# Performance work log

Measured on AMD Instinct MI355X. Metric: run time of the kernel, lower is better.

The kernel has to match this reference:

```python
import jax, jax.numpy as jnp
import numpy as np

N_Q = 16384; N_S = 16384; NN = 32; F_IN = 128; F_OUT = 256
K = 15; DIM = 3
RADIUS = 10.0
KP_EXTENT_CFG = 1.0      # config.NETWORK.KP_EXTENT (also scales learned offsets)
DENSITY = 5.0            # config.NETWORK.DENSITY_PARAMETER
EXTENT = KP_EXTENT_CFG * RADIUS / DENSITY   # 2.0
K_RADIUS = 1.5 * EXTENT
OFFSET_DIM = DIM * (K - 1)  # modulated=False, version=0 -> 42


def setup_inputs() -> dict:
    key = jax.random.key(0)
    ks = jax.random.split(key, 8)
    query_points = jax.random.uniform(ks[0], (N_Q, DIM), dtype=jnp.float32)
    support_points = jax.random.uniform(ks[1], (N_S, DIM), dtype=jnp.float32)
    neighbors = jax.random.randint(ks[2], (N_Q, NN), 0, N_S)
    features = jax.random.normal(ks[3], (N_S, F_IN), dtype=jnp.float32)
    # kernel points: fixed disposition inside ball of radius 1.5*extent, first point at center
    kp = jax.random.normal(ks[4], (K, DIM), dtype=jnp.float32)
    kp = kp / jnp.linalg.norm(kp, axis=1, keepdims=True) * (0.7 * K_RADIUS)
    K_points = kp.at[0].set(0.0)
    weight = jax.random.normal(ks[5], (K, F_IN, F_OUT), dtype=jnp.float32) / np.sqrt(F_IN)
    deformable_weight = jax.random.normal(ks[6], (K, F_IN, OFFSET_DIM), dtype=jnp.float32) / np.sqrt(F_IN)
    bias = jnp.zeros((OFFSET_DIM,), dtype=jnp.float32)
    return {"query_points": query_points, "support_points": support_points,
            "neighbors": neighbors, "features": features, "K_points": K_points,
            "weight": weight, "deformable_weight": deformable_weight, "bias": bias}


def _gather_neighb(query_points, support_points, neighbors, features):
    # pad with shadow point (far away) and zero feature row, as in KPConv_ops
    sp = jnp.concatenate([support_points, jnp.full((1, DIM), 1e6, support_points.dtype)], 0)
    ft = jnp.concatenate([features, jnp.zeros((1, features.shape[1]), features.dtype)], 0)
    rel = sp[neighbors] - query_points[:, None, :]   # [n, nn, 3]
    nfeat = ft[neighbors]                            # [n, nn, f]
    return rel, nfeat


def _linear_influence(sq_dist):
    # KP_INFLUENCE='linear': relu(1 - d/extent); CONVOLUTION_MODE='sum'
    return jnp.maximum(1.0 - jnp.sqrt(sq_dist) / EXTENT, 0.0)


def reference(query_points, support_points, neighbors, features, K_points,
              weight, deformable_weight, bias):
    rel, nfeat = _gather_neighb(query_points, support_points, neighbors, features)

    # --- rigid KPConv producing offsets (version=0) ---
    d0 = rel[:, :, None, :] - K_points[None, None, :, :]   # [n, nn, K, 3]
    sq0 = jnp.sum(d0 * d0, axis=-1)                        # [n, nn, K]
    w0 = _linear_influence(sq0)
    wf0 = jnp.einsum('enk,enf->ekf', w0, nfeat)            # [n, K, f]
    feat0 = jnp.einsum('ekf,kfo->eo', wf0, deformable_weight) + bias  # [n, 42]

    # not modulated: reshape to offsets, prepend zero offset for center kernel point
    offsets = feat0.reshape(-1, K - 1, DIM)
    offsets = jnp.concatenate([jnp.zeros_like(offsets[:, :1, :]), offsets], axis=1)
    offsets = offsets * KP_EXTENT_CFG                      # [n, K, 3]

    # --- deformable KPConv ---
    def_kp = K_points[None, :, :] + offsets                # [n, K, 3]
    d1 = rel[:, :, None, :] - def_kp[:, None, :, :]        # [n, nn, K, 3]
    sq1 = jnp.sum(d1 * d1, axis=-1)                        # [n, nn, K]
    w1 = _linear_influence(sq1)                            # out-of-range neighbors get 0 weight
    wf1 = jnp.einsum('enk,enf->ekf', w1, nfeat)            # [n, K, f]
    out = jnp.einsum('ekf,kfo->eo', wf1, weight)           # [n, f_out]
    return out
```

## Files before the change

kernel.cpp:

```cpp
#include <hip/hip_runtime.h>
#include <hip/hip_bf16.h>
#include <math.h>

typedef __attribute__((ext_vector_type(8))) short bf16x8;
typedef __attribute__((ext_vector_type(4))) float f32x4;

#define NQ 16384
#define NN 32
#define FI 128
#define FO 256
#define KPN 15
#define OD 42
#define INV_EXT 0.5f

#define KT2 64
#define WST 2048

#define SWZ(row, blk) (((blk) ^ ((row) & 7)) << 5)

#define WS_FP1    0u
#define WS_FP2    (8u * 1024u * 1024u)
#define WS_BSW    (12u * 1024u * 1024u)
#define WS_DWBH   (13u * 1024u * 1024u)
#define WS_DWBL   (WS_DWBH + 196608u)
#define WS_DEFKP  (14u * 1024u * 1024u)

static __device__ __forceinline__ unsigned short f2bf(float x) {
    union { __hip_bfloat16 h; unsigned short u; } cv;
    cv.h = __float2bfloat16(x);
    return cv.u;
}
static __device__ __forceinline__ float bf2f(unsigned short h) {
    union { unsigned int u; float f; } cv;
    cv.u = ((unsigned int)h) << 16;
    return cv.f;
}

__global__ void pre_all(const float* __restrict__ feat,
                        unsigned int* __restrict__ fp1, unsigned int* __restrict__ fp2,
                        const float* __restrict__ w, unsigned short* __restrict__ Bsw,
                        const float* __restrict__ dw,
                        unsigned short* __restrict__ dhi, unsigned short* __restrict__ dlo)
{
    const int b = blockIdx.x, t = threadIdx.x;
    if (b < 4096) {
        const int tid = b * 256 + t;
        const int s = tid >> 6, r = tid & 63;
        const int fp = r >> 4, low = r & 15;
        const float a = feat[s * FI + fp * 32 + low];
        const float c = feat[s * FI + fp * 32 + 16 + low];
        const unsigned short ha = f2bf(a), hc = f2bf(c);
        const unsigned int w0 = (unsigned int)ha | ((unsigned int)hc << 16);
        const unsigned int w1 = (unsigned int)f2bf(a - bf2f(ha)) |
                                ((unsigned int)f2bf(c - bf2f(hc)) << 16);
        uint2 pr; pr.x = w0; pr.y = w1;
        *(uint2*)&fp1[s * 128 + fp * 32 + low * 2] = pr;
        fp2[s * 64 + fp * 16 + low] = w0;
    } else if (b < 4096 + 256) {
        const int tid = (b - 4096) * 256 + t;
        const int lane = tid & 63;
        const int kt   = (tid >> 6) & 63;
        const int nt   = tid >> 12;
        const int n    = nt * 16 + (lane & 15);
        const int kbase = kt * 32 + (lane >> 4) * 8;
        unsigned int p[4];
        #pragma unroll
        for (int jj = 0; jj < 4; jj++) {
            unsigned int lo, hi;
            {
                const int kk = kbase + 2 * jj;
                const int f = kk >> 4, k = kk & 15;
                lo = (k < KPN) ? f2bf(w[(k * FI + f) * FO + n]) : 0u;
            }
            {
                const int kk = kbase + 2 * jj + 1;
                const int f = kk >> 4, k = kk & 15;
                hi = (k < KPN) ? f2bf(w[(k * FI + f) * FO + n]) : 0u;
            }
            p[jj] = lo | (hi << 16);
        }
        unsigned int* op = (unsigned int*)&Bsw[tid * 8];
        op[0] = p[0]; op[1] = p[1]; op[2] = p[2]; op[3] = p[3];
    } else {
        const int tid = (b - 4352) * 256 + t;
        const int lane = tid & 63;
        const int kt   = (tid >> 6) & 63;
        const int nt   = tid >> 12;
        const int o    = nt * 16 + (lane & 15);
        const int kbase = kt * 32 + (lane >> 4) * 8;
        #pragma unroll
        for (int j = 0; j < 8; j++) {
            const int kf = kbase + j;
            const int f = kf >> 4, k = kf & 15;
            float v = (k < KPN && o < OD) ? dw[(k * FI + f) * OD + o] : 0.f;
            unsigned short h = f2bf(v);
            dhi[tid * 8 + j] = h;
            dlo[tid * 8 + j] = f2bf(v - bf2f(h));
        }
    }
}

__global__ __launch_bounds__(512, 4)
void k1_offsets(const float* __restrict__ query, const float* __restrict__ support,
                const int* __restrict__ neighbors, const unsigned int* __restrict__ fp1,
                const float* __restrict__ kpoints,
                const unsigned short* __restrict__ dwB_hi,
                const unsigned short* __restrict__ dwB_lo,
                const float* __restrict__ bias, float* __restrict__ defkp)
{
    __shared__ unsigned short wfA_hi[8 * WST];
    __shared__ unsigned short wfA_lo[8 * WST];
    __shared__ float relx[256], rely[256], relz[256];
    __shared__ int   nbr_s[256];
    __shared__ float kp_s[48];
    __shared__ f32x4 cred[3 * 64];

    const int t = threadIdx.x;
    const int qbase = blockIdx.x * 8;
    if (t < 45) kp_s[t] = kpoints[t];
    if (t >= 45 && t < 48) kp_s[t] = 0.f;

    if (t < 256) {
        const int e = t >> 5, n = t & 31;
        const int q = qbase + e;
        const int idx = neighbors[q * NN + n];
        nbr_s[t] = idx;
        relx[t] = support[idx * 3 + 0] - query[q * 3 + 0];
        rely[t] = support[idx * 3 + 1] - query[q * 3 + 1];
        relz[t] = support[idx * 3 + 2] - query[q * 3 + 2];
    }
    __syncthreads();

    const int wave = t >> 6, lane = t & 63;
    const int quad = lane >> 4, low = lane & 15;

    {
        const int ee = wave;
        const int kb = (low < KPN) ? low * 3 : 0;
        const float kx = kp_s[kb + 0], ky = kp_s[kb + 1], kz = kp_s[kb + 2];
        union { unsigned short u[8]; bf16x8 v; } ah, al;
        int rows[8];
        #pragma unroll
        for (int j = 0; j < 8; j++) {
            const int ni = ee * 32 + quad * 8 + j;
            rows[j] = nbr_s[ni];
            const float dx = relx[ni] - kx;
            const float dy = rely[ni] - ky;
            const float dz = relz[ni] - kz;
            const float d = sqrtf(dx * dx + dy * dy + dz * dz);
            float w = 1.0f - d * INV_EXT;
            w = (low < KPN && w > 0.f) ? w : 0.f;
            const unsigned short h = f2bf(w);
            ah.u[j] = h;
            al.u[j] = f2bf(w - bf2f(h));
        }
        #pragma unroll
        for (int fp = 0; fp < 4; fp++) {
            union { unsigned int u[4]; bf16x8 v; } bhA, blA, bhB, blB;
            #pragma unroll
            for (int jj = 0; jj < 4; jj++) {
                const uint2 d0 = *(const uint2*)&fp1[rows[2 * jj] * 128 + fp * 32 + low * 2];
                const uint2 d1 = *(const uint2*)&fp1[rows[2 * jj + 1] * 128 + fp * 32 + low * 2];
                bhA.u[jj] = __builtin_amdgcn_perm(d1.x, d0.x, 0x05040100u);
                bhB.u[jj] = __builtin_amdgcn_perm(d1.x, d0.x, 0x07060302u);
                blA.u[jj] = __builtin_amdgcn_perm(d1.y, d0.y, 0x05040100u);
                blB.u[jj] = __builtin_amdgcn_perm(d1.y, d0.y, 0x07060302u);
            }
            #pragma unroll
            for (int hh2 = 0; hh2 < 2; hh2++) {
                const bf16x8 bh = hh2 ? bhB.v : bhA.v;
                const bf16x8 bl = hh2 ? blB.v : blA.v;
                const int ft = fp * 2 + hh2;
                f32x4 acc = {0.f, 0.f, 0.f, 0.f};
                acc = __builtin_amdgcn_mfma_f32_16x16x32_bf16(al.v, bh, acc, 0, 0, 0);
                acc = __builtin_amdgcn_mfma_f32_16x16x32_bf16(ah.v, bl, acc, 0, 0, 0);
                acc = __builtin_amdgcn_mfma_f32_16x16x32_bf16(ah.v, bh, acc, 0, 0, 0);
                const int col  = ft * 16 + low;
                const int base = ee * WST + SWZ(ee, col >> 1) + ((col & 1) << 4) + quad * 4;
                const unsigned short h0 = f2bf(acc[0]), h1 = f2bf(acc[1]);
                const unsigned short h2 = f2bf(acc[2]), h3 = f2bf(acc[3]);
                unsigned int* ph = (unsigned int*)&wfA_hi[base];
                ph[0] = (unsigned int)h0 | ((unsigned int)h1 << 16);
                ph[1] = (unsigned int)h2 | ((unsigned int)h3 << 16);
                unsigned int* pl = (unsigned int*)&wfA_lo[base];
                pl[0] = (unsigned int)f2bf(acc[0] - bf2f(h0)) |
                        ((unsigned int)f2bf(acc[1] - bf2f(h1)) << 16);
                pl[1] = (unsigned int)f2bf(acc[2] - bf2f(h2)) |
                        ((unsigned int)f2bf(acc[3] - bf2f(h3)) << 16);
            }
        }
    }
    __syncthreads();

    f32x4 acc = {0.f, 0.f, 0.f, 0.f};
    const int nt = wave >> 1, half = wave & 1;
    if (wave < 6) {
        const bf16x8* Bh = (const bf16x8*)dwB_hi;
        const bf16x8* Bl = (const bf16x8*)dwB_lo;
        const int rl = low & 7;
        const int arow = rl * WST;
        const int kt0 = half * 32;
        #pragma unroll 2
        for (int kt = kt0; kt < kt0 + 32; kt++) {
            const int ao = arow + SWZ(rl, kt) + quad * 8;
            bf16x8 a_h = *(const bf16x8*)&wfA_hi[ao];
            bf16x8 a_l = *(const bf16x8*)&wfA_lo[ao];
            bf16x8 b_h = Bh[(nt * KT2 + kt) * 64 + lane];
            bf16x8 b_l = Bl[(nt * KT2 + kt) * 64 + lane];
            acc = __builtin_amdgcn_mfma_f32_16x16x32_bf16(a_l, b_h, acc, 0, 0, 0);
            acc = __builtin_amdgcn_mfma_f32_16x16x32_bf16(a_h, b_l, acc, 0, 0, 0);
            acc = __builtin_amdgcn_mfma_f32_16x16x32_bf16(a_h, b_h, acc, 0, 0, 0);
        }
        if (half == 1) cred[nt * 64 + lane] = acc;
    } else if (wave == 6 && lane < 24) {
        defkp[(qbase + lane / 3) * 45 + (lane % 3)] = kp_s[lane % 3];
    }
    __syncthreads();

    if (wave < 6 && half == 0) {
        f32x4 o2 = cred[nt * 64 + lane];
        acc[0] += o2[0]; acc[1] += o2[1]; acc[2] += o2[2]; acc[3] += o2[3];
        const int o = nt * 16 + low;
        if (quad < 2 && o < OD) {
            const float bo = bias[o] + kp_s[3 + o];
            #pragma unroll
            for (int r = 0; r < 4; r++) {
                const int ee = quad * 4 + r;
                defkp[(qbase + ee) * 45 + 3 + o] = bo + acc[r];
            }
        }
    }
}

__global__ __launch_bounds__(512, 4)
void k2_deform(const float* __restrict__ query, const float* __restrict__ support,
               const int* __restrict__ neighbors, const unsigned int* __restrict__ fp2,
               const unsigned short* __restrict__ Bsw, const float* __restrict__ defkp,
               float* __restrict__ out)
{
    __shared__ unsigned short wfA[16 * WST];
    __shared__ float relx[512], rely[512], relz[512];
    __shared__ float dk_s[16 * 45];
    __shared__ int   nbr_s[512];

    const int t = threadIdx.x;
    const int qbase = blockIdx.x * 16;

    for (int i = t; i < 16 * 45; i += 512) dk_s[i] = defkp[qbase * 45 + i];

    const int e = t >> 5, n = t & 31;
    const int q = qbase + e;
    const int idx = neighbors[q * NN + n];
    nbr_s[t] = idx;
    relx[t] = support[idx * 3 + 0] - query[q * 3 + 0];
    rely[t] = support[idx * 3 + 1] - query[q * 3 + 1];
    relz[t] = support[idx * 3 + 2] - query[q * 3 + 2];
    __syncthreads();

    const int wave = t >> 6, lane = t & 63;
    const int quad = lane >> 4, low = lane & 15;

    {
        const int kb = (low < KPN) ? low * 3 : 0;
        for (int ei = 0; ei < 2; ei++) {
            const int ee = wave * 2 + ei;
            const float kx = dk_s[ee * 45 + kb + 0];
            const float ky = dk_s[ee * 45 + kb + 1];
            const float kz = dk_s[ee * 45 + kb + 2];
            union { unsigned short u[8]; bf16x8 v; } a;
            int rows[8];
            #pragma unroll
            for (int j = 0; j < 8; j++) {
                const int ni = ee * 32 + quad * 8 + j;
                rows[j] = nbr_s[ni];
                const float dx = relx[ni] - kx;
                const float dy = rely[ni] - ky;
                const float dz = relz[ni] - kz;
                const float d = sqrtf(dx * dx + dy * dy + dz * dz);
                float w = 1.0f - d * INV_EXT;
                w = (low < KPN && w > 0.f) ? w : 0.f;
                a.u[j] = f2bf(w);
            }
            #pragma unroll
            for (int fp = 0; fp < 4; fp++) {
                union { unsigned int u[4]; bf16x8 v; } bA, bB;
                #pragma unroll
                for (int jj = 0; jj < 4; jj++) {
                    const unsigned int d0 = fp2[rows[2 * jj] * 64 + fp * 16 + low];
                    const unsigned int d1 = fp2[rows[2 * jj + 1] * 64 + fp * 16 + low];
                    bA.u[jj] = __builtin_amdgcn_perm(d1, d0, 0x05040100u);
                    bB.u[jj] = __builtin_amdgcn_perm(d1, d0, 0x07060302u);
                }
                #pragma unroll
                for (int hh2 = 0; hh2 < 2; hh2++) {
                    const bf16x8 b = hh2 ? bB.v : bA.v;
                    const int ft = fp * 2 + hh2;
                    f32x4 acc = {0.f, 0.f, 0.f, 0.f};
                    acc = __builtin_amdgcn_mfma_f32_16x16x32_bf16(a.v, b, acc, 0, 0, 0);
                    const int col  = ft * 16 + low;
                    const int base = ee * WST + SWZ(ee, col >> 1) + ((col & 1) << 4) + quad * 4;
                    unsigned int* wp = (unsigned int*)&wfA[base];
                    wp[0] = (unsigned int)f2bf(acc[0]) | ((unsigned int)f2bf(acc[1]) << 16);
                    wp[1] = (unsigned int)f2bf(acc[2]) | ((unsigned int)f2bf(acc[3]) << 16);
                }
            }
        }
    }
    __syncthreads();

    {
        const int nt0 = wave * 2, nt1 = nt0 + 1;
        f32x4 acc0 = {0.f, 0.f, 0.f, 0.f}, acc1 = {0.f, 0.f, 0.f, 0.f};
        const bf16x8* Bp = (const bf16x8*)Bsw;
        const int arow = low * WST;
        #pragma unroll 4
        for (int kt = 0; kt < KT2; kt++) {
            bf16x8 a  = *(const bf16x8*)&wfA[arow + SWZ(low, kt) + quad * 8];
            bf16x8 b0 = Bp[(nt0 * KT2 + kt) * 64 + lane];
            bf16x8 b1 = Bp[(nt1 * KT2 + kt) * 64 + lane];
            acc0 = __builtin_amdgcn_mfma_f32_16x16x32_bf16(a, b0, acc0, 0, 0, 0);
            acc1 = __builtin_amdgcn_mfma_f32_16x16x32_bf16(a, b1, acc1, 0, 0, 0);
        }
        #pragma unroll
        for (int r = 0; r < 4; r++) {
            const int ee = quad * 4 + r;
            out[(qbase + ee) * FO + nt0 * 16 + low] = acc0[r];
            out[(qbase + ee) * FO + nt1 * 16 + low] = acc1[r];
        }
    }
}

extern "C" void kernel_launch(void* const* d_in, const int* in_sizes, int n_in,
                              void* d_out, int out_size, void* d_ws, size_t ws_size,
                              hipStream_t stream) {
    const float* query     = (const float*)d_in[0];
    const float* support   = (const float*)d_in[1];
    const int*   neighbors = (const int*)  d_in[2];
    const float* features  = (const float*)d_in[3];
    const float* kpoints   = (const float*)d_in[4];
    const float* weight    = (const float*)d_in[5];
    const float* dweight   = (const float*)d_in[6];
    const float* bias      = (const float*)d_in[7];
    float*       out       = (float*)d_out;

    char* ws = (char*)d_ws;
    unsigned int*   fp1  = (unsigned int*)(ws + WS_FP1);
    unsigned int*   fp2  = (unsigned int*)(ws + WS_FP2);
    unsigned short* Bsw  = (unsigned short*)(ws + WS_BSW);
    unsigned short* dwBh = (unsigned short*)(ws + WS_DWBH);
    unsigned short* dwBl = (unsigned short*)(ws + WS_DWBL);
    float*          defkp = (float*)(ws + WS_DEFKP);

    pre_all<<<4400, 256, 0, stream>>>(features, fp1, fp2, weight, Bsw,
                                      dweight, dwBh, dwBl);
    k1_offsets<<<NQ / 8, 512, 0, stream>>>(query, support, neighbors, fp1,
                                           kpoints, dwBh, dwBl, bias, defkp);
    k2_deform<<<NQ / 16, 512, 0, stream>>>(query, support, neighbors, fp2,
                                           Bsw, defkp, out);
}
```

Measured before the change: 190.8 us.

## Double queries per block and chunk the K-dimension through shared memory

Both the offset and deformable kernels now handle twice as many query points per block (16 and 32). The weighted-feature A tile is produced and consumed in four K-chunks with a new transposed, XOR-swizzled LDS layout, so the LDS footprint stays bounded while each weight B-fragment loaded from global memory is reused across more query rows. In the deform kernel every wave now uses the full 16-row MFMA M dimension twice instead of padding, and neighbor indices are stored as 16-bit values. The cost is extra barriers per chunk, more registers for the additional accumulators, and fewer blocks in flight.

```diff
diff --git a/kernel.cpp b/kernel.cpp
--- a/kernel.cpp
+++ b/kernel.cpp
@@ -13,11 +13,6 @@
 #define OD 42
 #define INV_EXT 0.5f
 
-#define KT2 64
-#define WST 2048
-
-#define SWZ(row, blk) (((blk) ^ ((row) & 7)) << 5)
-
 #define WS_FP1    0u
 #define WS_FP2    (8u * 1024u * 1024u)
 #define WS_BSW    (12u * 1024u * 1024u)
@@ -35,6 +30,8 @@
     cv.u = ((unsigned int)h) << 16;
     return cv.f;
 }
+
+union U8 { unsigned short u[8]; bf16x8 v; };
 
 __global__ void pre_all(const float* __restrict__ feat,
                         unsigned int* __restrict__ fp1, unsigned int* __restrict__ fp2,
@@ -108,19 +105,19 @@
                 const unsigned short* __restrict__ dwB_lo,
                 const float* __restrict__ bias, float* __restrict__ defkp)
 {
-    __shared__ unsigned short wfA_hi[8 * WST];
-    __shared__ unsigned short wfA_lo[8 * WST];
-    __shared__ float relx[256], rely[256], relz[256];
-    __shared__ int   nbr_s[256];
+    __shared__ unsigned short wfA_hi[8192];
+    __shared__ unsigned short wfA_lo[8192];
+    __shared__ float relx[512], rely[512], relz[512];
+    __shared__ int   nbr_s[512];
     __shared__ float kp_s[48];
     __shared__ f32x4 cred[3 * 64];
 
     const int t = threadIdx.x;
-    const int qbase = blockIdx.x * 8;
+    const int qbase = blockIdx.x * 16;
     if (t < 45) kp_s[t] = kpoints[t];
     if (t >= 45 && t < 48) kp_s[t] = 0.f;
 
-    if (t < 256) {
+    {
         const int e = t >> 5, n = t & 31;
         const int q = qbase + e;
         const int idx = neighbors[q * NN + n];
@@ -133,17 +130,16 @@
 
     const int wave = t >> 6, lane = t & 63;
     const int quad = lane >> 4, low = lane & 15;
-
-    {
-        const int ee = wave;
-        const int kb = (low < KPN) ? low * 3 : 0;
-        const float kx = kp_s[kb + 0], ky = kp_s[kb + 1], kz = kp_s[kb + 2];
-        union { unsigned short u[8]; bf16x8 v; } ah, al;
-        int rows[8];
+    const int ee0 = wave * 2;
+
+    const int kb = (low < KPN) ? low * 3 : 0;
+    const float kx = kp_s[kb + 0], ky = kp_s[kb + 1], kz = kp_s[kb + 2];
+    U8 ah[2], al[2];
+    #pragma unroll
+    for (int ei = 0; ei < 2; ei++) {
         #pragma unroll
         for (int j = 0; j < 8; j++) {
-            const int ni = ee * 32 + quad * 8 + j;
-            rows[j] = nbr_s[ni];
+            const int ni = (ee0 + ei) * 32 + quad * 8 + j;
             const float dx = relx[ni] - kx;
             const float dy = rely[ni] - ky;
             const float dz = relz[ni] - kz;
@@ -151,16 +147,25 @@
             float w = 1.0f - d * INV_EXT;
             w = (low < KPN && w > 0.f) ? w : 0.f;
             const unsigned short h = f2bf(w);
-            ah.u[j] = h;
-            al.u[j] = f2bf(w - bf2f(h));
-        }
-        #pragma unroll
-        for (int fp = 0; fp < 4; fp++) {
+            ah[ei].u[j] = h;
+            al[ei].u[j] = f2bf(w - bf2f(h));
+        }
+    }
+
+    f32x4 acc = {0.f, 0.f, 0.f, 0.f};
+    const int nt = wave >> 1, half = wave & 1;
+
+    for (int c = 0; c < 4; c++) {
+        #pragma unroll
+        for (int ei = 0; ei < 2; ei++) {
+            const int ee = ee0 + ei;
             union { unsigned int u[4]; bf16x8 v; } bhA, blA, bhB, blB;
             #pragma unroll
             for (int jj = 0; jj < 4; jj++) {
-                const uint2 d0 = *(const uint2*)&fp1[rows[2 * jj] * 128 + fp * 32 + low * 2];
-                const uint2 d1 = *(const uint2*)&fp1[rows[2 * jj + 1] * 128 + fp * 32 + low * 2];
+                const int r0 = nbr_s[ee * 32 + quad * 8 + 2 * jj];
+                const int r1 = nbr_s[ee * 32 + quad * 8 + 2 * jj + 1];
+                const uint2 d0 = *(const uint2*)&fp1[r0 * 128 + c * 32 + low * 2];
+                const uint2 d1 = *(const uint2*)&fp1[r1 * 128 + c * 32 + low * 2];
                 bhA.u[jj] = __builtin_amdgcn_perm(d1.x, d0.x, 0x05040100u);
                 bhB.u[jj] = __builtin_amdgcn_perm(d1.x, d0.x, 0x07060302u);
                 blA.u[jj] = __builtin_amdgcn_perm(d1.y, d0.y, 0x05040100u);
@@ -170,58 +175,56 @@
             for (int hh2 = 0; hh2 < 2; hh2++) {
                 const bf16x8 bh = hh2 ? bhB.v : bhA.v;
                 const bf16x8 bl = hh2 ? blB.v : blA.v;
-                const int ft = fp * 2 + hh2;
-                f32x4 acc = {0.f, 0.f, 0.f, 0.f};
-                acc = __builtin_amdgcn_mfma_f32_16x16x32_bf16(al.v, bh, acc, 0, 0, 0);
-                acc = __builtin_amdgcn_mfma_f32_16x16x32_bf16(ah.v, bl, acc, 0, 0, 0);
-                acc = __builtin_amdgcn_mfma_f32_16x16x32_bf16(ah.v, bh, acc, 0, 0, 0);
-                const int col  = ft * 16 + low;
-                const int base = ee * WST + SWZ(ee, col >> 1) + ((col & 1) << 4) + quad * 4;
-                const unsigned short h0 = f2bf(acc[0]), h1 = f2bf(acc[1]);
-                const unsigned short h2 = f2bf(acc[2]), h3 = f2bf(acc[3]);
-                unsigned int* ph = (unsigned int*)&wfA_hi[base];
-                ph[0] = (unsigned int)h0 | ((unsigned int)h1 << 16);
-                ph[1] = (unsigned int)h2 | ((unsigned int)h3 << 16);
-                unsigned int* pl = (unsigned int*)&wfA_lo[base];
-                pl[0] = (unsigned int)f2bf(acc[0] - bf2f(h0)) |
-                        ((unsigned int)f2bf(acc[1] - bf2f(h1)) << 16);
-                pl[1] = (unsigned int)f2bf(acc[2] - bf2f(h2)) |
-                        ((unsigned int)f2bf(acc[3] - bf2f(h3)) << 16);
-            }
-        }
-    }
+                f32x4 o = {0.f, 0.f, 0.f, 0.f};
+                o = __builtin_amdgcn_mfma_f32_16x16x32_bf16(al[ei].v, bh, o, 0, 0, 0);
+                o = __builtin_amdgcn_mfma_f32_16x16x32_bf16(ah[ei].v, bl, o, 0, 0, 0);
+                o = __builtin_amdgcn_mfma_f32_16x16x32_bf16(ah[ei].v, bh, o, 0, 0, 0);
+                const int cblk = (hh2 * 16 + low) * 2 + (quad >> 1);
+                const int hw = cblk * 128 + ((ee ^ (cblk & 15)) * 8) + (quad & 1) * 4;
+                const unsigned short h0 = f2bf(o[0]), h1 = f2bf(o[1]);
+                const unsigned short h2 = f2bf(o[2]), h3 = f2bf(o[3]);
+                uint2 ph;
+                ph.x = (unsigned int)h0 | ((unsigned int)h1 << 16);
+                ph.y = (unsigned int)h2 | ((unsigned int)h3 << 16);
+                *(uint2*)&wfA_hi[hw] = ph;
+                uint2 pl;
+                pl.x = (unsigned int)f2bf(o[0] - bf2f(h0)) |
+                       ((unsigned int)f2bf(o[1] - bf2f(h1)) << 16);
+                pl.y = (unsigned int)f2bf(o[2] - bf2f(h2)) |
+                       ((unsigned int)f2bf(o[3] - bf2f(h3)) << 16);
+                *(uint2*)&wfA_lo[hw] = pl;
+            }
+        }
+        __syncthreads();
+        if (wave < 6) {
+            const bf16x8* Bh = (const bf16x8*)dwB_hi;
+            const bf16x8* Bl = (const bf16x8*)dwB_lo;
+            #pragma unroll 4
+            for (int ktl = half * 8; ktl < half * 8 + 8; ktl++) {
+                const int cblk = ktl * 4 + quad;
+                const int hw = cblk * 128 + ((low ^ (cblk & 15)) * 8);
+                bf16x8 a_h = *(const bf16x8*)&wfA_hi[hw];
+                bf16x8 a_l = *(const bf16x8*)&wfA_lo[hw];
+                const int ktg = c * 16 + ktl;
+                bf16x8 b_h = Bh[(nt * 64 + ktg) * 64 + lane];
+                bf16x8 b_l = Bl[(nt * 64 + ktg) * 64 + lane];
+                acc = __builtin_amdgcn_mfma_f32_16x16x32_bf16(a_l, b_h, acc, 0, 0, 0);
+                acc = __builtin_amdgcn_mfma_f32_16x16x32_bf16(a_h, b_l, acc, 0, 0, 0);
+                acc = __builtin_amdgcn_mfma_f32_16x16x32_bf16(a_h, b_h, acc, 0, 0, 0);
+            }
+        } else if (c == 0 && wave == 6 && lane < 48) {
+            defkp[(qbase + lane / 3) * 45 + (lane % 3)] = kp_s[lane % 3];
+        }
+        __syncthreads();
+    }
+
+    if (wave < 6 && half == 1) cred[nt * 64 + lane] = acc;
     __syncthreads();
-
-    f32x4 acc = {0.f, 0.f, 0.f, 0.f};
-    const int nt = wave >> 1, half = wave & 1;
-    if (wave < 6) {
-        const bf16x8* Bh = (const bf16x8*)dwB_hi;
-        const bf16x8* Bl = (const bf16x8*)dwB_lo;
-        const int rl = low & 7;
-        const int arow = rl * WST;
-        const int kt0 = half * 32;
-        #pragma unroll 2
-        for (int kt = kt0; kt < kt0 + 32; kt++) {
-            const int ao = arow + SWZ(rl, kt) + quad * 8;
-            bf16x8 a_h = *(const bf16x8*)&wfA_hi[ao];
-            bf16x8 a_l = *(const bf16x8*)&wfA_lo[ao];
-            bf16x8 b_h = Bh[(nt * KT2 + kt) * 64 + lane];
-            bf16x8 b_l = Bl[(nt * KT2 + kt) * 64 + lane];
-            acc = __builtin_amdgcn_mfma_f32_16x16x32_bf16(a_l, b_h, acc, 0, 0, 0);
-            acc = __builtin_amdgcn_mfma_f32_16x16x32_bf16(a_h, b_l, acc, 0, 0, 0);
-            acc = __builtin_amdgcn_mfma_f32_16x16x32_bf16(a_h, b_h, acc, 0, 0, 0);
-        }
-        if (half == 1) cred[nt * 64 + lane] = acc;
-    } else if (wave == 6 && lane < 24) {
-        defkp[(qbase + lane / 3) * 45 + (lane % 3)] = kp_s[lane % 3];
-    }
-    __syncthreads();
-
     if (wave < 6 && half == 0) {
         f32x4 o2 = cred[nt * 64 + lane];
         acc[0] += o2[0]; acc[1] += o2[1]; acc[2] += o2[2]; acc[3] += o2[3];
         const int o = nt * 16 + low;
-        if (quad < 2 && o < OD) {
+        if (o < OD) {
             const float bo = bias[o] + kp_s[3 + o];
             #pragma unroll
             for (int r = 0; r < 4; r++) {
@@ -238,95 +241,111 @@
                const unsigned short* __restrict__ Bsw, const float* __restrict__ defkp,
                float* __restrict__ out)
 {
-    __shared__ unsigned short wfA[16 * WST];
-    __shared__ float relx[512], rely[512], relz[512];
-    __shared__ float dk_s[16 * 45];
-    __shared__ int   nbr_s[512];
+    __shared__ unsigned short wfA[16384];
+    __shared__ float relx[1024], rely[1024], relz[1024];
+    __shared__ float dk_s[32 * 45];
+    __shared__ unsigned short nbr_s[1024];
 
     const int t = threadIdx.x;
-    const int qbase = blockIdx.x * 16;
-
-    for (int i = t; i < 16 * 45; i += 512) dk_s[i] = defkp[qbase * 45 + i];
-
-    const int e = t >> 5, n = t & 31;
-    const int q = qbase + e;
-    const int idx = neighbors[q * NN + n];
-    nbr_s[t] = idx;
-    relx[t] = support[idx * 3 + 0] - query[q * 3 + 0];
-    rely[t] = support[idx * 3 + 1] - query[q * 3 + 1];
-    relz[t] = support[idx * 3 + 2] - query[q * 3 + 2];
+    const int qbase = blockIdx.x * 32;
+
+    for (int i = t; i < 32 * 45; i += 512) dk_s[i] = defkp[qbase * 45 + i];
+    #pragma unroll
+    for (int ii = 0; ii < 2; ii++) {
+        const int i = ii * 512 + t;
+        const int e = i >> 5, n = i & 31;
+        const int q = qbase + e;
+        const int idx = neighbors[q * NN + n];
+        nbr_s[i] = (unsigned short)idx;
+        relx[i] = support[idx * 3 + 0] - query[q * 3 + 0];
+        rely[i] = support[idx * 3 + 1] - query[q * 3 + 1];
+        relz[i] = support[idx * 3 + 2] - query[q * 3 + 2];
+    }
     __syncthreads();
 
     const int wave = t >> 6, lane = t & 63;
     const int quad = lane >> 4, low = lane & 15;
-
-    {
-        const int kb = (low < KPN) ? low * 3 : 0;
-        for (int ei = 0; ei < 2; ei++) {
-            const int ee = wave * 2 + ei;
-            const float kx = dk_s[ee * 45 + kb + 0];
-            const float ky = dk_s[ee * 45 + kb + 1];
-            const float kz = dk_s[ee * 45 + kb + 2];
-            union { unsigned short u[8]; bf16x8 v; } a;
-            int rows[8];
-            #pragma unroll
-            for (int j = 0; j < 8; j++) {
-                const int ni = ee * 32 + quad * 8 + j;
-                rows[j] = nbr_s[ni];
-                const float dx = relx[ni] - kx;
-                const float dy = rely[ni] - ky;
-                const float dz = relz[ni] - kz;
-                const float d = sqrtf(dx * dx + dy * dy + dz * dz);
-                float w = 1.0f - d * INV_EXT;
-                w = (low < KPN && w > 0.f) ? w : 0.f;
-                a.u[j] = f2bf(w);
-            }
-            #pragma unroll
-            for (int fp = 0; fp < 4; fp++) {
-                union { unsigned int u[4]; bf16x8 v; } bA, bB;
-                #pragma unroll
-                for (int jj = 0; jj < 4; jj++) {
-                    const unsigned int d0 = fp2[rows[2 * jj] * 64 + fp * 16 + low];
-                    const unsigned int d1 = fp2[rows[2 * jj + 1] * 64 + fp * 16 + low];
-                    bA.u[jj] = __builtin_amdgcn_perm(d1, d0, 0x05040100u);
-                    bB.u[jj] = __builtin_amdgcn_perm(d1, d0, 0x07060302u);
-                }
-                #pragma unroll
-                for (int hh2 = 0; hh2 < 2; hh2++) {
-                    const bf16x8 b = hh2 ? bB.v : bA.v;
-                    const int ft = fp * 2 + hh2;
-                    f32x4 acc = {0.f, 0.f, 0.f, 0.f};
-                    acc = __builtin_amdgcn_mfma_f32_16x16x32_bf16(a.v, b, acc, 0, 0, 0);
-                    const int col  = ft * 16 + low;
-                    const int base = ee * WST + SWZ(ee, col >> 1) + ((col & 1) << 4) + quad * 4;
-                    unsigned int* wp = (unsigned int*)&wfA[base];
-                    wp[0] = (unsigned int)f2bf(acc[0]) | ((unsigned int)f2bf(acc[1]) << 16);
-                    wp[1] = (unsigned int)f2bf(acc[2]) | ((unsigned int)f2bf(acc[3]) << 16);
-                }
-            }
-        }
-    }
-    __syncthreads();
-
-    {
-        const int nt0 = wave * 2, nt1 = nt0 + 1;
-        f32x4 acc0 = {0.f, 0.f, 0.f, 0.f}, acc1 = {0.f, 0.f, 0.f, 0.f};
-        const bf16x8* Bp = (const bf16x8*)Bsw;
-        const int arow = low * WST;
+    const int ee0 = wave * 4;
+    const int kb = (low < KPN) ? low * 3 : 0;
+
+    U8 af[4];
+    #pragma unroll
+    for (int ei = 0; ei < 4; ei++) {
+        const int ee = ee0 + ei;
+        const float kx = dk_s[ee * 45 + kb + 0];
+        const float ky = dk_s[ee * 45 + kb + 1];
+        const float kz = dk_s[ee * 45 + kb + 2];
+        #pragma unroll
+        for (int j = 0; j < 8; j++) {
+            const int ni = ee * 32 + quad * 8 + j;
+            const float dx = relx[ni] - kx;
+            const float dy = rely[ni] - ky;
+            const float dz = relz[ni] - kz;
+            const float d = sqrtf(dx * dx + dy * dy + dz * dz);
+            float w = 1.0f - d * INV_EXT;
+            w = (low < KPN && w > 0.f) ? w : 0.f;
+            af[ei].u[j] = f2bf(w);
+        }
+    }
+
+    f32x4 acc00 = {0,0,0,0}, acc01 = {0,0,0,0};
+    f32x4 acc10 = {0,0,0,0}, acc11 = {0,0,0,0};
+    const int nt0 = wave * 2, nt1 = nt0 + 1;
+    const bf16x8* Bp = (const bf16x8*)Bsw;
+
+    for (int c = 0; c < 4; c++) {
+        #pragma unroll
+        for (int ei = 0; ei < 4; ei++) {
+            const int ee = ee0 + ei;
+            union { unsigned int u[4]; bf16x8 v; } bA, bB;
+            #pragma unroll
+            for (int jj = 0; jj < 4; jj++) {
+                const int r0 = nbr_s[ee * 32 + quad * 8 + 2 * jj];
+                const int r1 = nbr_s[ee * 32 + quad * 8 + 2 * jj + 1];
+                const unsigned int d0 = fp2[r0 * 64 + c * 16 + low];
+                const unsigned int d1 = fp2[r1 * 64 + c * 16 + low];
+                bA.u[jj] = __builtin_amdgcn_perm(d1, d0, 0x05040100u);
+                bB.u[jj] = __builtin_amdgcn_perm(d1, d0, 0x07060302u);
+            }
+            #pragma unroll
+            for (int hh2 = 0; hh2 < 2; hh2++) {
+                const bf16x8 b = hh2 ? bB.v : bA.v;
+                f32x4 o = {0.f, 0.f, 0.f, 0.f};
+                o = __builtin_amdgcn_mfma_f32_16x16x32_bf16(af[ei].v, b, o, 0, 0, 0);
+                const int cblk = (hh2 * 16 + low) * 2 + (quad >> 1);
+                const int hw = cblk * 256 + ((ee ^ (cblk & 31)) * 8) + (quad & 1) * 4;
+                uint2 ph;
+                ph.x = (unsigned int)f2bf(o[0]) | ((unsigned int)f2bf(o[1]) << 16);
+                ph.y = (unsigned int)f2bf(o[2]) | ((unsigned int)f2bf(o[3]) << 16);
+                *(uint2*)&wfA[hw] = ph;
+            }
+        }
+        __syncthreads();
         #pragma unroll 4
-        for (int kt = 0; kt < KT2; kt++) {
-            bf16x8 a  = *(const bf16x8*)&wfA[arow + SWZ(low, kt) + quad * 8];
-            bf16x8 b0 = Bp[(nt0 * KT2 + kt) * 64 + lane];
-            bf16x8 b1 = Bp[(nt1 * KT2 + kt) * 64 + lane];
-            acc0 = __builtin_amdgcn_mfma_f32_16x16x32_bf16(a, b0, acc0, 0, 0, 0);
-            acc1 = __builtin_amdgcn_mfma_f32_16x16x32_bf16(a, b1, acc1, 0, 0, 0);
-        }
-        #pragma unroll
-        for (int r = 0; r < 4; r++) {
-            const int ee = quad * 4 + r;
-            out[(qbase + ee) * FO + nt0 * 16 + low] = acc0[r];
-            out[(qbase + ee) * FO + nt1 * 16 + low] = acc1[r];
-        }
+        for (int ktl = 0; ktl < 16; ktl++) {
+            const int cblk = ktl * 4 + quad;
+            const int s0 = (low ^ (cblk & 31)) * 8;
+            const int s1 = ((16 + low) ^ (cblk & 31)) * 8;
+            bf16x8 a0 = *(const bf16x8*)&wfA[cblk * 256 + s0];
+            bf16x8 a1 = *(const bf16x8*)&wfA[cblk * 256 + s1];
+            const int ktg = c * 16 + ktl;
+            bf16x8 b0 = Bp[(nt0 * 64 + ktg) * 64 + lane];
+            bf16x8 b1 = Bp[(nt1 * 64 + ktg) * 64 + lane];
+            acc00 = __builtin_amdgcn_mfma_f32_16x16x32_bf16(a0, b0, acc00, 0, 0, 0);
+            acc01 = __builtin_amdgcn_mfma_f32_16x16x32_bf16(a0, b1, acc01, 0, 0, 0);
+            acc10 = __builtin_amdgcn_mfma_f32_16x16x32_bf16(a1, b0, acc10, 0, 0, 0);
+            acc11 = __builtin_amdgcn_mfma_f32_16x16x32_bf16(a1, b1, acc11, 0, 0, 0);
+        }
+        __syncthreads();
+    }
+
+    #pragma unroll
+    for (int r = 0; r < 4; r++) {
+        const int e0 = quad * 4 + r;
+        out[(qbase + e0) * FO + nt0 * 16 + low] = acc00[r];
+        out[(qbase + e0) * FO + nt1 * 16 + low] = acc01[r];
+        out[(qbase + 16 + e0) * FO + nt0 * 16 + low] = acc10[r];
+        out[(qbase + 16 + e0) * FO + nt1 * 16 + low] = acc11[r];
     }
 }
 
@@ -353,8 +372,8 @@
 
     pre_all<<<4400, 256, 0, stream>>>(features, fp1, fp2, weight, Bsw,
                                       dweight, dwBh, dwBl);
-    k1_offsets<<<NQ / 8, 512, 0, stream>>>(query, support, neighbors, fp1,
-                                           kpoints, dwBh, dwBl, bias, defkp);
-    k2_deform<<<NQ / 16, 512, 0, stream>>>(query, support, neighbors, fp2,
+    k1_offsets<<<NQ / 16, 512, 0, stream>>>(query, support, neighbors, fp1,
+                                            kpoints, dwBh, dwBl, bias, defkp);
+    k2_deform<<<NQ / 32, 512, 0, stream>>>(query, support, neighbors, fp2,
                                            Bsw, defkp, out);
 }
```

New measurement: 167.7 us. 12.1% less time.
